# Optimization experiments

Hardware: AMD Instinct MI355X
Metric: run time of the kernel (lower is better)

## Reference

```python
import jax, jax.numpy as jnp
import numpy as np

B, INPUT_DIM, EMB_DIM = 16384, 2048, 768
DOMAIN_NUM, MEMORY_NUM, TAU = 9, 10, 32.0


def setup_inputs() -> dict:
    key = jax.random.key(0)
    k1, k2, k3, k4, k5 = jax.random.split(key, 5)
    feature = jax.random.normal(k1, (B, INPUT_DIM), dtype=jnp.float32)
    category = jax.random.randint(k2, (B,), 0, DOMAIN_NUM, dtype=jnp.int64)
    # Linear(input_dim, emb_dim, bias=False) weights: [emb_dim, input_dim]
    W_topic = jax.random.normal(k3, (EMB_DIM, INPUT_DIM), dtype=jnp.float32) * 0.02
    W_domain = jax.random.normal(k4, (EMB_DIM, INPUT_DIM), dtype=jnp.float32) * 0.02
    # domain_num Embedding(memory_num, emb_dim) tables, stacked: [D, M, E]
    memory_tables = jax.random.normal(k5, (DOMAIN_NUM, MEMORY_NUM, EMB_DIM), dtype=jnp.float32)
    return {"feature": feature, "W_topic": W_topic, "W_domain": W_domain,
            "memory_tables": memory_tables, "category": category}


def reference(feature, W_topic, W_domain, memory_tables, category):
    eps = 1e-12
    # F.normalize(feature, p=2, dim=-1)
    norm = jnp.maximum(jnp.linalg.norm(feature, axis=-1, keepdims=True), eps)
    feat = feature / norm                                   # [B, I]
    # per-sample gather of each sample's category memory table: [B, M, E]
    mem = memory_tables[category]
    # faithful quirk: loop over domain_num indexes the BATCH dim of the stack
    D = memory_tables.shape[0]
    mems_d = mem[:D]                                        # [D, M, E]
    t = feat @ W_topic.T                                    # [B, E]
    topic_att = jax.nn.softmax(jnp.einsum('be,dme->bdm', t, mems_d) * TAU, axis=-1)
    sep = jnp.einsum('bdm,dme->bde', topic_att, mems_d)     # [B, D, E]
    dproj = feat @ W_domain.T                               # [B, E]
    domain_att = jax.nn.softmax(jnp.einsum('bde,be->bd', sep, dproj) * TAU, axis=-1)
    return domain_att[:, None, :]                           # [B, 1, D]
```

## Files before the change

### kernel.cpp

```cpp
#include <hip/hip_runtime.h>
#include <math.h>

#define TAU_F 32.0f

typedef __attribute__((ext_vector_type(8))) _Float16 half8;
typedef __attribute__((ext_vector_type(2))) __fp16 half2v;
typedef __attribute__((ext_vector_type(4))) float f32x4;

union HU { uint4 u; half8 v; };

__global__ __launch_bounds__(256) void gproj2(
    const float* __restrict__ Wt, const float* __restrict__ Wd,
    const float* __restrict__ mem, const int* __restrict__ cat,
    float* __restrict__ P)
{
    __shared__ float Ml[96 * 36];
    __shared__ float Wl[32 * 68];

    const int bid = blockIdx.x;
    const int mat = bid >> 7;
    const int ks  = (bid >> 5) & 3;
    const int ct  = bid & 31;
    const int c0  = ct * 64;
    const int tid = threadIdx.x;
    const float* __restrict__ W = mat ? Wd : Wt;

    const int tr = tid >> 4;
    const int tc = tid & 15;

    float acc[6][4];
    #pragma unroll
    for (int j = 0; j < 6; ++j)
        #pragma unroll
        for (int q = 0; q < 4; ++q) acc[j][q] = 0.f;

    for (int ch = 0; ch < 6; ++ch) {
        __syncthreads();
        #pragma unroll
        for (int p = 0; p < 3; ++p) {
            const int idx = tid + 256 * p;
            const int r   = idx >> 3;
            const int kq  = idx & 7;
            float4 v = make_float4(0.f, 0.f, 0.f, 0.f);
            if (r < 90) {
                const int d = r / 10;
                const int mrow = cat[d] * 10 + (r - d * 10);
                v = *(const float4*)(mem + (size_t)mrow * 768 + ks * 192 + ch * 32 + kq * 4);
            }
            *(float4*)(Ml + r * 36 + kq * 4) = v;
        }
        #pragma unroll
        for (int p = 0; p < 2; ++p) {
            const int idx = tid + 256 * p;
            const int e   = idx >> 4;
            const int c4  = (idx & 15) * 4;
            *(float4*)(Wl + e * 68 + c4) =
                *(const float4*)(W + (size_t)(ks * 192 + ch * 32 + e) * 2048 + c0 + c4);
        }
        __syncthreads();

        #pragma unroll
        for (int e = 0; e < 32; e += 4) {
            float4 m4[6], w4[4];
            #pragma unroll
            for (int j = 0; j < 6; ++j) m4[j] = *(const float4*)(Ml + (tr * 6 + j) * 36 + e);
            #pragma unroll
            for (int q = 0; q < 4; ++q) w4[q] = *(const float4*)(Wl + (e + q) * 68 + tc * 4);
            #pragma unroll
            for (int j = 0; j < 6; ++j) {
                const float mv[4] = {m4[j].x, m4[j].y, m4[j].z, m4[j].w};
                #pragma unroll
                for (int q = 0; q < 4; ++q) {
                    acc[j][0] = fmaf(mv[q], w4[q].x, acc[j][0]);
                    acc[j][1] = fmaf(mv[q], w4[q].y, acc[j][1]);
                    acc[j][2] = fmaf(mv[q], w4[q].z, acc[j][2]);
                    acc[j][3] = fmaf(mv[q], w4[q].w, acc[j][3]);
                }
            }
        }
    }

    #pragma unroll
    for (int j = 0; j < 6; ++j) {
        float4 v = make_float4(acc[j][0], acc[j][1], acc[j][2], acc[j][3]);
        *(float4*)(P + (size_t)ks * 393216 + (size_t)(mat * 96 + tr * 6 + j) * 2048 + c0 + tc * 4) = v;
    }
}

__global__ __launch_bounds__(256) void split_g3(
    const float* __restrict__ P, unsigned short* __restrict__ gB)
{
    const int u  = blockIdx.x * 256 + threadIdx.x;
    const int n  = u >> 8;
    const int k0 = (u & 255) * 8;

    float s[8] = {0.f, 0.f, 0.f, 0.f, 0.f, 0.f, 0.f, 0.f};
    #pragma unroll
    for (int ks = 0; ks < 4; ++ks) {
        const float4 a = *(const float4*)(P + (size_t)ks * 393216 + (size_t)n * 2048 + k0);
        const float4 b = *(const float4*)(P + (size_t)ks * 393216 + (size_t)n * 2048 + k0 + 4);
        s[0] += a.x; s[1] += a.y; s[2] += a.z; s[3] += a.w;
        s[4] += b.x; s[5] += b.y; s[6] += b.z; s[7] += b.w;
    }
    union { _Float16 h[8]; uint4 u4; } hi, lo;
    #pragma unroll
    for (int e = 0; e < 8; ++e) {
        const _Float16 h = (_Float16)s[e];
        hi.h[e] = h;
        lo.h[e] = (_Float16)(s[e] - (float)h);
    }
    const int kc = k0 >> 5;
    const int lq = (k0 >> 3) & 3;
    const int nq = n / 48;
    const int rm = n - nq * 48;
    const int j  = rm >> 4;
    const int lm = rm & 15;
    const size_t fH = (size_t)((kc * 12 + nq * 3 + j) * 2 + 0) * 512 + lq * 128 + lm * 8;
    const size_t fL = (size_t)((kc * 12 + nq * 3 + j) * 2 + 1) * 512 + lq * 128 + lm * 8;
    *(uint4*)(gB + fH) = hi.u4;
    *(uint4*)(gB + fL) = lo.u4;
}

__global__ __launch_bounds__(256, 3) void fused_mfma5(
    const float* __restrict__ feat, const unsigned short* __restrict__ gB,
    float* __restrict__ P2, float* __restrict__ ssqp)
{
    __shared__ __align__(16) unsigned short aS[10240];

    const int tid = threadIdx.x;
    const int rt  = blockIdx.x >> 1;
    const int ks  = blockIdx.x & 1;
    const int row0 = rt * 64;

    const int nq = tid >> 6, l = tid & 63;
    const int lm = l & 15,  lq = l >> 4;
    const int r8 = tid >> 2, kq = tid & 3;

    f32x4 acc[4][3];
    #pragma unroll
    for (int i = 0; i < 4; ++i)
        #pragma unroll
        for (int j = 0; j < 3; ++j) acc[i][j] = (f32x4)0.f;
    float ssq = 0.f;

    const float* fbase = feat + (size_t)(row0 + r8) * 2048 + ks * 1024 + kq * 8;
    const unsigned short* bbase = gB + (size_t)ks * 393216 + (nq * 3) * 1024 + l * 8;

    float4 f0 = *(const float4*)(fbase);
    float4 f1 = *(const float4*)(fbase + 4);
    uint4 bh[3], bl[3];
    #pragma unroll
    for (int j = 0; j < 3; ++j) {
        bh[j] = *(const uint4*)(bbase + j * 1024);
        bl[j] = *(const uint4*)(bbase + j * 1024 + 512);
    }
    {
        const float xs[8] = {f0.x, f0.y, f0.z, f0.w, f1.x, f1.y, f1.z, f1.w};
        union { half2v h2[4]; uint4 u4; } uh, ul;
        #pragma unroll
        for (int e = 0; e < 4; ++e) {
            const float a = xs[2 * e], b = xs[2 * e + 1];
            ssq = fmaf(a, a, ssq); ssq = fmaf(b, b, ssq);
            half2v h = __builtin_amdgcn_cvt_pkrtz(a, b);
            uh.h2[e] = h;
            ul.h2[e] = __builtin_amdgcn_cvt_pkrtz(a - (float)h[0], b - (float)h[1]);
        }
        *(uint4*)(aS + 0 * 2560 + r8 * 40 + kq * 8) = uh.u4;
        *(uint4*)(aS + 1 * 2560 + r8 * 40 + kq * 8) = ul.u4;
    }
    float4 fn0 = *(const float4*)(fbase + 32);
    float4 fn1 = *(const float4*)(fbase + 36);
    __syncthreads();

    for (int kc = 0; kc < 32; ++kc) {
        const int ka = (kc + 2 < 32) ? kc + 2 : 31;
        float4 fa0 = *(const float4*)(fbase + ka * 32);
        float4 fa1 = *(const float4*)(fbase + ka * 32 + 4);
        const int kb = (kc + 1 < 32) ? kc + 1 : 31;
        uint4 bhn[3], bln[3];
        #pragma unroll
        for (int j = 0; j < 3; ++j) {
            bhn[j] = *(const uint4*)(bbase + (size_t)kb * 12288 + j * 1024);
            bln[j] = *(const uint4*)(bbase + (size_t)kb * 12288 + j * 1024 + 512);
        }

        if (kc < 31) {
            const int nb = (kc + 1) & 1;
            const float xs[8] = {fn0.x, fn0.y, fn0.z, fn0.w, fn1.x, fn1.y, fn1.z, fn1.w};
            union { half2v h2[4]; uint4 u4; } uh, ul;
            #pragma unroll
            for (int e = 0; e < 4; ++e) {
                const float a = xs[2 * e], b = xs[2 * e + 1];
                ssq = fmaf(a, a, ssq); ssq = fmaf(b, b, ssq);
                half2v h = __builtin_amdgcn_cvt_pkrtz(a, b);
                uh.h2[e] = h;
                ul.h2[e] = __builtin_amdgcn_cvt_pkrtz(a - (float)h[0], b - (float)h[1]);
            }
            *(uint4*)(aS + (nb * 2 + 0) * 2560 + r8 * 40 + kq * 8) = uh.u4;
            *(uint4*)(aS + (nb * 2 + 1) * 2560 + r8 * 40 + kq * 8) = ul.u4;
        }

        const int cb = kc & 1;
        const unsigned short* aH = aS + (cb * 2 + 0) * 2560;
        const unsigned short* aL = aS + (cb * 2 + 1) * 2560;
        half8 fh[4], fl[4];
        #pragma unroll
        for (int i = 0; i < 4; ++i) {
            HU th, tl;
            th.u = *(const uint4*)(aH + (i * 16 + lm) * 40 + lq * 8);
            tl.u = *(const uint4*)(aL + (i * 16 + lm) * 40 + lq * 8);
            fh[i] = th.v; fl[i] = tl.v;
        }
        #pragma unroll
        for (int j = 0; j < 3; ++j) {
            HU h8, l8; h8.u = bh[j]; l8.u = bl[j];
            #pragma unroll
            for (int i = 0; i < 4; ++i) {
                acc[i][j] = __builtin_amdgcn_mfma_f32_16x16x32_f16(fh[i], h8.v, acc[i][j], 0, 0, 0);
                acc[i][j] = __builtin_amdgcn_mfma_f32_16x16x32_f16(fh[i], l8.v, acc[i][j], 0, 0, 0);
                acc[i][j] = __builtin_amdgcn_mfma_f32_16x16x32_f16(fl[i], h8.v, acc[i][j], 0, 0, 0);
            }
        }
        __syncthreads();

        fn0 = fa0; fn1 = fa1;
        #pragma unroll
        for (int j = 0; j < 3; ++j) { bh[j] = bhn[j]; bl[j] = bln[j]; }
    }

    ssq += __shfl_xor(ssq, 1, 64);
    ssq += __shfl_xor(ssq, 2, 64);
    if ((tid & 3) == 0) ssqp[(size_t)ks * 16384 + row0 + (tid >> 2)] = ssq;

    #pragma unroll
    for (int i = 0; i < 4; ++i)
        #pragma unroll
        for (int j = 0; j < 3; ++j)
            #pragma unroll
            for (int r = 0; r < 4; ++r)
                P2[((size_t)ks * 16384 + row0 + i * 16 + lq * 4 + r) * 192 + nq * 48 + j * 16 + lm]
                    = acc[i][j][r];
}

#define EP_SPAD 196
__global__ __launch_bounds__(256) void ep_kernel(
    const float* __restrict__ P2, const float* __restrict__ ssqp,
    float* __restrict__ out)
{
    __shared__ float sc[64 * EP_SPAD];
    const int tid  = threadIdx.x;
    const int row0 = blockIdx.x * 64;

    float4 s[12];
    #pragma unroll
    for (int p = 0; p < 12; ++p) s[p] = make_float4(0.f, 0.f, 0.f, 0.f);
    #pragma unroll
    for (int ks = 0; ks < 2; ++ks)
        #pragma unroll
        for (int p = 0; p < 12; ++p) {
            const int u   = p * 256 + tid;
            const int row = u / 48;
            const int c4  = (u - row * 48) * 4;
            const float4 v = *(const float4*)(P2 + ((size_t)ks * 16384 + row0 + row) * 192 + c4);
            s[p].x += v.x; s[p].y += v.y; s[p].z += v.z; s[p].w += v.w;
        }
    #pragma unroll
    for (int p = 0; p < 12; ++p) {
        const int u   = p * 256 + tid;
        const int row = u / 48;
        const int c4  = (u - row * 48) * 4;
        *(float4*)(sc + row * EP_SPAD + c4) = s[p];
    }
    float nsq = 0.f;
    if (tid < 64) {
        nsq = ssqp[row0 + tid] + ssqp[16384 + row0 + tid];
    }
    __syncthreads();

    if (tid < 64) {
        const int r = tid;
        const float inv = TAU_F / fmaxf(sqrtf(nsq), 1e-12f);
        const float* scr = sc + (size_t)r * EP_SPAD;
        float lg[9];
        float dmax = -1e30f;
        #pragma unroll
        for (int d = 0; d < 9; ++d) {
            const float* v = scr + d * 10;
            const float* u = scr + 96 + d * 10;
            float mx = v[0];
            #pragma unroll
            for (int m = 1; m < 10; ++m) mx = fmaxf(mx, v[m]);
            float ssum = 0.f, dot = 0.f;
            #pragma unroll
            for (int m = 0; m < 10; ++m) {
                const float p = __expf((v[m] - mx) * inv);
                ssum += p;
                dot = fmaf(p, u[m], dot);
            }
            const float lgt = (dot / ssum) * inv;
            lg[d] = lgt;
            dmax = fmaxf(dmax, lgt);
        }
        float s2 = 0.f;
        #pragma unroll
        for (int d = 0; d < 9; ++d) { const float p = __expf(lg[d] - dmax); lg[d] = p; s2 += p; }
        const float r2 = 1.0f / s2;
        #pragma unroll
        for (int d = 0; d < 9; ++d)
            out[(size_t)(row0 + r) * 9 + d] = lg[d] * r2;
    }
}

extern "C" void kernel_launch(void* const* d_in, const int* in_sizes, int n_in,
                              void* d_out, int out_size, void* d_ws, size_t ws_size,
                              hipStream_t stream) {
    const float* feature = (const float*)d_in[0];
    const float* Wt      = (const float*)d_in[1];
    const float* Wd      = (const float*)d_in[2];
    const float* mem     = (const float*)d_in[3];
    const int*   cat     = (const int*)d_in[4];

    float* P2 = (float*)d_ws;
    float* P  = (float*)d_ws;
    unsigned short* gB = (unsigned short*)((char*)d_ws + 50331648);
    float* ssqp = (float*)((char*)d_ws + 50331648 + 1572864);
    float* out = (float*)d_out;

    gproj2<<<256, 256, 0, stream>>>(Wt, Wd, mem, cat, P);
    split_g3<<<192, 256, 0, stream>>>(P, gB);
    fused_mfma5<<<512, 256, 0, stream>>>(feature, gB, P2, ssqp);
    ep_kernel<<<256, 256, 0, stream>>>(P2, ssqp, out);
}
```

Measured before the change: 257.0 us.

## Use single-pass fp16 MFMA for domain columns and stagger wave column order

The fused MFMA kernel now runs the three-pass split-fp16 product only for the topic half of the output columns. The domain half uses a single hi×hi MFMA and skips loading the lo weights and lo activations for it. Waves rotate their column quarter by block index, the LDS row pitch changes to 44, the barrier waits only on LDS counters, and occupancy drops to 2 blocks. This cuts MFMA work and loads on the domain path but lowers its accuracy, creates divergence between waves, and relies on the custom barrier being safe.

Result: faster. 250.1 us (-2.7%).

```diff
diff --git a/kernel.cpp b/kernel.cpp
--- a/kernel.cpp
+++ b/kernel.cpp
@@ -8,6 +8,11 @@
 typedef __attribute__((ext_vector_type(4))) float f32x4;
 
 union HU { uint4 u; half8 v; };
+
+__device__ __forceinline__ void sync_lds_only() {
+    asm volatile("s_waitcnt lgkmcnt(0)" ::: "memory");
+    __builtin_amdgcn_s_barrier();
+}
 
 __global__ __launch_bounds__(256) void gproj2(
     const float* __restrict__ Wt, const float* __restrict__ Wd,
@@ -121,19 +126,21 @@
     *(uint4*)(gB + fL) = lo.u4;
 }
 
-__global__ __launch_bounds__(256, 3) void fused_mfma5(
+__global__ __launch_bounds__(256, 2) void fused_mfma6(
     const float* __restrict__ feat, const unsigned short* __restrict__ gB,
     float* __restrict__ P2, float* __restrict__ ssqp)
 {
-    __shared__ __align__(16) unsigned short aS[10240];
+    __shared__ __align__(16) unsigned short aS[4 * 64 * 44];
 
     const int tid = threadIdx.x;
     const int rt  = blockIdx.x >> 1;
     const int ks  = blockIdx.x & 1;
     const int row0 = rt * 64;
 
-    const int nq = tid >> 6, l = tid & 63;
+    const int w  = tid >> 6, l = tid & 63;
     const int lm = l & 15,  lq = l >> 4;
+    const int nq = (w + blockIdx.x) & 3;
+    const bool topic = (nq < 2);
     const int r8 = tid >> 2, kq = tid & 3;
 
     f32x4 acc[4][3];
@@ -144,18 +151,22 @@
     float ssq = 0.f;
 
     const float* fbase = feat + (size_t)(row0 + r8) * 2048 + ks * 1024 + kq * 8;
-    const unsigned short* bbase = gB + (size_t)ks * 393216 + (nq * 3) * 1024 + l * 8;
-
-    float4 f0 = *(const float4*)(fbase);
-    float4 f1 = *(const float4*)(fbase + 4);
+    const unsigned short* bbase = gB + (size_t)ks * 393216 + nq * 3072 + l * 8;
+
+    float4 c0a = *(const float4*)(fbase);
+    float4 c0b = *(const float4*)(fbase + 4);
+    float4 c1a = *(const float4*)(fbase + 32);
+    float4 c1b = *(const float4*)(fbase + 36);
     uint4 bh[3], bl[3];
     #pragma unroll
-    for (int j = 0; j < 3; ++j) {
-        bh[j] = *(const uint4*)(bbase + j * 1024);
-        bl[j] = *(const uint4*)(bbase + j * 1024 + 512);
-    }
-    {
-        const float xs[8] = {f0.x, f0.y, f0.z, f0.w, f1.x, f1.y, f1.z, f1.w};
+    for (int j = 0; j < 3; ++j) bh[j] = *(const uint4*)(bbase + j * 1024);
+    if (topic) {
+        #pragma unroll
+        for (int j = 0; j < 3; ++j) bl[j] = *(const uint4*)(bbase + j * 1024 + 512);
+    }
+
+    auto cw = [&](int buf, float4 va, float4 vb) {
+        const float xs[8] = {va.x, va.y, va.z, va.w, vb.x, vb.y, vb.z, vb.w};
         union { half2v h2[4]; uint4 u4; } uh, ul;
         #pragma unroll
         for (int e = 0; e < 4; ++e) {
@@ -165,72 +176,82 @@
             uh.h2[e] = h;
             ul.h2[e] = __builtin_amdgcn_cvt_pkrtz(a - (float)h[0], b - (float)h[1]);
         }
-        *(uint4*)(aS + 0 * 2560 + r8 * 40 + kq * 8) = uh.u4;
-        *(uint4*)(aS + 1 * 2560 + r8 * 40 + kq * 8) = ul.u4;
-    }
-    float4 fn0 = *(const float4*)(fbase + 32);
-    float4 fn1 = *(const float4*)(fbase + 36);
-    __syncthreads();
+        *(uint4*)(aS + (size_t)((buf * 2 + 0) * 64 + r8) * 44 + kq * 8) = uh.u4;
+        *(uint4*)(aS + (size_t)((buf * 2 + 1) * 64 + r8) * 44 + kq * 8) = ul.u4;
+    };
+
+    cw(0, c0a, c0b);
+    sync_lds_only();
 
     for (int kc = 0; kc < 32; ++kc) {
-        const int ka = (kc + 2 < 32) ? kc + 2 : 31;
-        float4 fa0 = *(const float4*)(fbase + ka * 32);
-        float4 fa1 = *(const float4*)(fbase + ka * 32 + 4);
         const int kb = (kc + 1 < 32) ? kc + 1 : 31;
         uint4 bhn[3], bln[3];
         #pragma unroll
-        for (int j = 0; j < 3; ++j) {
+        for (int j = 0; j < 3; ++j)
             bhn[j] = *(const uint4*)(bbase + (size_t)kb * 12288 + j * 1024);
-            bln[j] = *(const uint4*)(bbase + (size_t)kb * 12288 + j * 1024 + 512);
-        }
-
-        if (kc < 31) {
-            const int nb = (kc + 1) & 1;
-            const float xs[8] = {fn0.x, fn0.y, fn0.z, fn0.w, fn1.x, fn1.y, fn1.z, fn1.w};
-            union { half2v h2[4]; uint4 u4; } uh, ul;
-            #pragma unroll
-            for (int e = 0; e < 4; ++e) {
-                const float a = xs[2 * e], b = xs[2 * e + 1];
-                ssq = fmaf(a, a, ssq); ssq = fmaf(b, b, ssq);
-                half2v h = __builtin_amdgcn_cvt_pkrtz(a, b);
-                uh.h2[e] = h;
-                ul.h2[e] = __builtin_amdgcn_cvt_pkrtz(a - (float)h[0], b - (float)h[1]);
-            }
-            *(uint4*)(aS + (nb * 2 + 0) * 2560 + r8 * 40 + kq * 8) = uh.u4;
-            *(uint4*)(aS + (nb * 2 + 1) * 2560 + r8 * 40 + kq * 8) = ul.u4;
-        }
+        if (topic) {
+            #pragma unroll
+            for (int j = 0; j < 3; ++j)
+                bln[j] = *(const uint4*)(bbase + (size_t)kb * 12288 + j * 1024 + 512);
+        }
+        const int ka = (kc + 2 < 32) ? kc + 2 : 31;
+        float4 cna = *(const float4*)(fbase + ka * 32);
+        float4 cnb = *(const float4*)(fbase + ka * 32 + 4);
+
+        if (kc < 31) cw((kc + 1) & 1, c1a, c1b);
 
         const int cb = kc & 1;
-        const unsigned short* aH = aS + (cb * 2 + 0) * 2560;
-        const unsigned short* aL = aS + (cb * 2 + 1) * 2560;
         half8 fh[4], fl[4];
         #pragma unroll
         for (int i = 0; i < 4; ++i) {
-            HU th, tl;
-            th.u = *(const uint4*)(aH + (i * 16 + lm) * 40 + lq * 8);
-            tl.u = *(const uint4*)(aL + (i * 16 + lm) * 40 + lq * 8);
-            fh[i] = th.v; fl[i] = tl.v;
-        }
-        #pragma unroll
-        for (int j = 0; j < 3; ++j) {
-            HU h8, l8; h8.u = bh[j]; l8.u = bl[j];
+            HU th;
+            th.u = *(const uint4*)(aS + (size_t)((cb * 2 + 0) * 64 + i * 16 + lm) * 44 + lq * 8);
+            fh[i] = th.v;
+        }
+        if (topic) {
             #pragma unroll
             for (int i = 0; i < 4; ++i) {
-                acc[i][j] = __builtin_amdgcn_mfma_f32_16x16x32_f16(fh[i], h8.v, acc[i][j], 0, 0, 0);
-                acc[i][j] = __builtin_amdgcn_mfma_f32_16x16x32_f16(fh[i], l8.v, acc[i][j], 0, 0, 0);
-                acc[i][j] = __builtin_amdgcn_mfma_f32_16x16x32_f16(fl[i], h8.v, acc[i][j], 0, 0, 0);
-            }
-        }
-        __syncthreads();
-
-        fn0 = fa0; fn1 = fa1;
-        #pragma unroll
-        for (int j = 0; j < 3; ++j) { bh[j] = bhn[j]; bl[j] = bln[j]; }
+                HU tl;
+                tl.u = *(const uint4*)(aS + (size_t)((cb * 2 + 1) * 64 + i * 16 + lm) * 44 + lq * 8);
+                fl[i] = tl.v;
+            }
+        }
+
+        if (topic) {
+            #pragma unroll
+            for (int j = 0; j < 3; ++j) {
+                HU h8, l8; h8.u = bh[j]; l8.u = bl[j];
+                #pragma unroll
+                for (int i = 0; i < 4; ++i) {
+                    acc[i][j] = __builtin_amdgcn_mfma_f32_16x16x32_f16(fh[i], h8.v, acc[i][j], 0, 0, 0);
+                    acc[i][j] = __builtin_amdgcn_mfma_f32_16x16x32_f16(fh[i], l8.v, acc[i][j], 0, 0, 0);
+                    acc[i][j] = __builtin_amdgcn_mfma_f32_16x16x32_f16(fl[i], h8.v, acc[i][j], 0, 0, 0);
+                }
+            }
+        } else {
+            #pragma unroll
+            for (int j = 0; j < 3; ++j) {
+                HU h8; h8.u = bh[j];
+                #pragma unroll
+                for (int i = 0; i < 4; ++i)
+                    acc[i][j] = __builtin_amdgcn_mfma_f32_16x16x32_f16(fh[i], h8.v, acc[i][j], 0, 0, 0);
+            }
+        }
+
+        sync_lds_only();
+
+        c1a = cna; c1b = cnb;
+        #pragma unroll
+        for (int j = 0; j < 3; ++j) bh[j] = bhn[j];
+        if (topic) {
+            #pragma unroll
+            for (int j = 0; j < 3; ++j) bl[j] = bln[j];
+        }
     }
 
     ssq += __shfl_xor(ssq, 1, 64);
     ssq += __shfl_xor(ssq, 2, 64);
-    if ((tid & 3) == 0) ssqp[(size_t)ks * 16384 + row0 + (tid >> 2)] = ssq;
+    if (kq == 0) ssqp[(size_t)ks * 16384 + row0 + r8] = ssq;
 
     #pragma unroll
     for (int i = 0; i < 4; ++i)
@@ -328,6 +349,6 @@
 
     gproj2<<<256, 256, 0, stream>>>(Wt, Wd, mem, cat, P);
     split_g3<<<192, 256, 0, stream>>>(P, gB);
-    fused_mfma5<<<512, 256, 0, stream>>>(feature, gB, P2, ssqp);
+    fused_mfma6<<<512, 256, 0, stream>>>(feature, gB, P2, ssqp);
     ep_kernel<<<256, 256, 0, stream>>>(P2, ssqp, out);
 }
```
